# Optimization experiments

Hardware: AMD Instinct MI355X
Metric: run time of the kernel (lower is better)

## Reference

```python
import jax, jax.numpy as jnp
import numpy as np


def _decode(fm):
    # fm: [B, A, H, W, 5+C] YOLO head output
    B, A, H, W, D = fm.shape
    box = fm[..., :4].reshape(B, -1, 4)
    conf = jax.nn.sigmoid(fm[..., 4].reshape(B, -1))
    cls = jax.nn.sigmoid(fm[..., 5:].reshape(B, -1, D - 5))
    # Faithful to the torch in-place sequence:
    #   b0 = (b0 - b2/2)*W ; b1 = (b1 - b3/2)*H
    #   b2 = (NEW b0 + OLD b2/2)*W ; b3 = (NEW b1 + OLD b3/2)*H
    w = jnp.asarray(W, fm.dtype)
    h = jnp.asarray(H, fm.dtype)
    x1 = (box[..., 0] - box[..., 2] / 2) * w
    y1 = (box[..., 1] - box[..., 3] / 2) * h
    x2 = (x1 + box[..., 2] / 2) * w
    y2 = (y1 + box[..., 3] / 2) * h
    boxes = jnp.stack([x1, y1, x2, y2], axis=-1)  # [B, A*H*W, 4]
    return boxes, conf, cls


def setup_inputs() -> dict:
    key = jax.random.key(0)
    k0, k1, k2, k3 = jax.random.split(key, 4)
    B, A, C = 16, 3, 80
    fm0 = jax.random.uniform(k0, (B, A, 80, 80, 5 + C), dtype=jnp.float32)
    fm1 = jax.random.uniform(k1, (B, A, 40, 40, 5 + C), dtype=jnp.float32)
    fm2 = jax.random.uniform(k2, (B, A, 20, 20, 5 + C), dtype=jnp.float32)
    detection_targets = jax.random.uniform(k3, (1, 4), dtype=jnp.float32)
    return {"fm0": fm0, "fm1": fm1, "fm2": fm2,
            "detection_targets": detection_targets}


def reference(fm0, fm1, fm2, detection_targets):
    boxes, scores, classes = [], [], []
    for fm in (fm0, fm1, fm2):
        b, s, c = _decode(fm)
        boxes.append(b)
        scores.append(s)
        classes.append(c)
    all_boxes = jnp.concatenate(boxes, axis=1)    # [B, N, 4]
    all_scores = jnp.concatenate(scores, axis=1)  # [B, N]
    all_classes = jnp.concatenate(classes, axis=1)  # [B, N, C]
    # Pack like the torch nms_input: [x1, y1, x2, y2, conf, cls...]
    return jnp.concatenate(
        [all_boxes, all_scores[..., None], all_classes], axis=-1)  # [B, N, 5+C]
```

## Files before the change

kernel.cpp:

```cpp
#include <hip/hip_runtime.h>

#define NB        16
#define NROWS_OUT 25200
#define L0_FLOATS 26112000
#define L1_FLOATS 6528000
#define L2_FLOATS 1632000
#define TOTAL_FLOATS (L0_FLOATS + L1_FLOATS + L2_FLOATS)
#define TOTAL4 (TOTAL_FLOATS / 4)

__device__ __forceinline__ float sigmoidf(float x) {
    return 1.0f / (1.0f + __expf(-x));
}

template <int ROWS, int OFF, int SCALE>
__device__ __forceinline__ void process4(const float* __restrict__ in,
                                         float* __restrict__ out,
                                         int f_local) {
    constexpr int ROWS85 = ROWS * 85;
    const int b   = f_local / ROWS85;
    const int rem = f_local - b * ROWS85;
    const int c0  = rem % 85;
    const float* src = in + f_local;
    const float4 x = *(const float4*)src;
    const int out_f = (b * NROWS_OUT + OFF) * 85 + rem;

    float xv[4] = {x.x, x.y, x.z, x.w};
    float y[4];
#pragma unroll
    for (int k = 0; k < 4; ++k) {
        int c = c0 + k;
        if (c >= 85) c -= 85;
        if (c >= 4) {
            y[k] = sigmoidf(xv[k]);
        } else {
            const float* row = src + (k - c);
            const float b0 = row[0], b1 = row[1], b2 = row[2], b3 = row[3];
            const float h2 = 0.5f * b2, h3 = 0.5f * b3;
            const float sc = (float)SCALE;
            const float x1 = (b0 - h2) * sc;
            const float y1 = (b1 - h3) * sc;
            float r;
            if (c == 0)      r = x1;
            else if (c == 1) r = y1;
            else if (c == 2) r = (x1 + h2) * sc;
            else             r = (y1 + h3) * sc;
            y[k] = r;
        }
    }
    *(float4*)(out + out_f) = make_float4(y[0], y[1], y[2], y[3]);
}

__global__ __launch_bounds__(256) void yolo_decode_kernel(
    const float* __restrict__ fm0, const float* __restrict__ fm1,
    const float* __restrict__ fm2, float* __restrict__ out) {
    const int v = blockIdx.x * 256 + threadIdx.x;
    if (v >= TOTAL4) return;
    const int f = v * 4;
    if (f < L0_FLOATS) {
        process4<19200, 0, 80>(fm0, out, f);
    } else if (f < L0_FLOATS + L1_FLOATS) {
        process4<4800, 19200, 40>(fm1, out, f - L0_FLOATS);
    } else {
        process4<1200, 24000, 20>(fm2, out, f - (L0_FLOATS + L1_FLOATS));
    }
}

extern "C" void kernel_launch(void* const* d_in, const int* in_sizes, int n_in,
                              void* d_out, int out_size, void* d_ws, size_t ws_size,
                              hipStream_t stream) {
    const float* fm0 = (const float*)d_in[0];
    const float* fm1 = (const float*)d_in[1];
    const float* fm2 = (const float*)d_in[2];
    float* out = (float*)d_out;

    const int blocks = (TOTAL4 + 255) / 256;
    hipLaunchKernelGGL(yolo_decode_kernel, dim3(blocks), dim3(256), 0, stream,
                       fm0, fm1, fm2, out);
}
```

Baseline: 252.8 us.

## Branchless decode with nontemporal stores and two float4 per thread

Replaces the divergent per-element box branch with an unconditional load of the nearest row's four box values, computes box outputs and sigmoid for every lane, and selects between them. Uses the hardware reciprocal for the sigmoid and nontemporal stores for the streaming output. Each thread now handles two float4 chunks half the array apart, halving the grid. These changes aim to cut divergence and cache pollution in a memory-bound copy, at the cost of extra scalar loads and redundant exp work on every element.

```diff
diff --git a/kernel.cpp b/kernel.cpp
--- a/kernel.cpp
+++ b/kernel.cpp
@@ -1,15 +1,18 @@
 #include <hip/hip_runtime.h>
 
-#define NB        16
 #define NROWS_OUT 25200
 #define L0_FLOATS 26112000
 #define L1_FLOATS 6528000
 #define L2_FLOATS 1632000
 #define TOTAL_FLOATS (L0_FLOATS + L1_FLOATS + L2_FLOATS)
-#define TOTAL4 (TOTAL_FLOATS / 4)
+#define TOTAL4   (TOTAL_FLOATS / 4)
+#define HALF4    (TOTAL4 / 2)
 
-__device__ __forceinline__ float sigmoidf(float x) {
-    return 1.0f / (1.0f + __expf(-x));
+typedef float v4f __attribute__((ext_vector_type(4)));
+
+__device__ __forceinline__ float fast_sigmoid(float x) {
+    float e = __expf(-x);
+    return __builtin_amdgcn_rcpf(1.0f + e);
 }
 
 template <int ROWS, int OFF, int SCALE>
@@ -20,9 +23,23 @@
     const int b   = f_local / ROWS85;
     const int rem = f_local - b * ROWS85;
     const int c0  = rem % 85;
-    const float* src = in + f_local;
-    const float4 x = *(const float4*)src;
-    const int out_f = (b * NROWS_OUT + OFF) * 85 + rem;
+
+    int g = f_local;
+    if (c0 <= 3)  g = f_local - c0;
+    if (c0 >= 82) g = f_local + (85 - c0);
+
+    const v4f x = *(const v4f*)(in + f_local);
+    const float r0 = in[g + 0];
+    const float r1 = in[g + 1];
+    const float r2 = in[g + 2];
+    const float r3 = in[g + 3];
+
+    const float sc = (float)SCALE;
+    const float h2 = 0.5f * r2, h3 = 0.5f * r3;
+    const float q0 = (r0 - h2) * sc;
+    const float q1 = (r1 - h3) * sc;
+    const float q2 = (q0 + h2) * sc;
+    const float q3 = (q1 + h3) * sc;
 
     float xv[4] = {x.x, x.y, x.z, x.w};
     float y[4];
@@ -30,32 +47,20 @@
     for (int k = 0; k < 4; ++k) {
         int c = c0 + k;
         if (c >= 85) c -= 85;
-        if (c >= 4) {
-            y[k] = sigmoidf(xv[k]);
-        } else {
-            const float* row = src + (k - c);
-            const float b0 = row[0], b1 = row[1], b2 = row[2], b3 = row[3];
-            const float h2 = 0.5f * b2, h3 = 0.5f * b3;
-            const float sc = (float)SCALE;
-            const float x1 = (b0 - h2) * sc;
-            const float y1 = (b1 - h3) * sc;
-            float r;
-            if (c == 0)      r = x1;
-            else if (c == 1) r = y1;
-            else if (c == 2) r = (x1 + h2) * sc;
-            else             r = (y1 + h3) * sc;
-            y[k] = r;
-        }
+        const float s = fast_sigmoid(xv[k]);
+        const float q = (c == 0) ? q0 : ((c == 1) ? q1 : ((c == 2) ? q2 : q3));
+        y[k] = (c < 4) ? q : s;
     }
-    *(float4*)(out + out_f) = make_float4(y[0], y[1], y[2], y[3]);
+
+    const int out_f = (b * NROWS_OUT + OFF) * 85 + rem;
+    v4f yo; yo.x = y[0]; yo.y = y[1]; yo.z = y[2]; yo.w = y[3];
+    __builtin_nontemporal_store(yo, (v4f*)(out + out_f));
 }
 
-__global__ __launch_bounds__(256) void yolo_decode_kernel(
-    const float* __restrict__ fm0, const float* __restrict__ fm1,
-    const float* __restrict__ fm2, float* __restrict__ out) {
-    const int v = blockIdx.x * 256 + threadIdx.x;
-    if (v >= TOTAL4) return;
-    const int f = v * 4;
+__device__ __forceinline__ void dispatch4(const float* __restrict__ fm0,
+                                          const float* __restrict__ fm1,
+                                          const float* __restrict__ fm2,
+                                          float* __restrict__ out, int f) {
     if (f < L0_FLOATS) {
         process4<19200, 0, 80>(fm0, out, f);
     } else if (f < L0_FLOATS + L1_FLOATS) {
@@ -63,6 +68,15 @@
     } else {
         process4<1200, 24000, 20>(fm2, out, f - (L0_FLOATS + L1_FLOATS));
     }
+}
+
+__global__ __launch_bounds__(256) void yolo_decode_kernel(
+    const float* __restrict__ fm0, const float* __restrict__ fm1,
+    const float* __restrict__ fm2, float* __restrict__ out) {
+    const int v = blockIdx.x * 256 + threadIdx.x;
+    if (v >= HALF4) return;
+    dispatch4(fm0, fm1, fm2, out, v * 4);
+    dispatch4(fm0, fm1, fm2, out, (v + HALF4) * 4);
 }
 
 extern "C" void kernel_launch(void* const* d_in, const int* in_sizes, int n_in,
@@ -73,7 +87,7 @@
     const float* fm2 = (const float*)d_in[2];
     float* out = (float*)d_out;
 
-    const int blocks = (TOTAL4 + 255) / 256;
+    const int blocks = (HALF4 + 255) / 256;
     hipLaunchKernelGGL(yolo_decode_kernel, dim3(blocks), dim3(256), 0, stream,
                        fm0, fm1, fm2, out);
 }
```

Result: faster. 237.0 us (-6.3%).
